# Performance work log

Hardware: AMD Instinct MI355X
Metric: run time of the kernel (lower is better)

Reference implementation:

```python
import jax, jax.numpy as jnp
import numpy as np

B, S, D, H = 2, 2048, 1024, 16
DK = D // H


def setup_inputs() -> dict:
    key = jax.random.key(0)
    ks = jax.random.split(key, 7)
    scale = 1.0 / np.sqrt(D)
    return {
        "q": jax.random.normal(ks[0], (B, S, D), dtype=jnp.float32),
        "k": jax.random.normal(ks[1], (B, S, D), dtype=jnp.float32),
        "v": jax.random.normal(ks[2], (B, S, D), dtype=jnp.float32),
        "mask": jnp.ones((B, 1, 1, S), dtype=jnp.int32),
        "Wq": (jax.random.normal(ks[3], (D, D), dtype=jnp.float32) * scale),
        "Wk": (jax.random.normal(ks[4], (D, D), dtype=jnp.float32) * scale),
        "Wv": (jax.random.normal(ks[5], (D, D), dtype=jnp.float32) * scale),
        "Wo": (jax.random.normal(ks[6], (D, D), dtype=jnp.float32) * scale),
    }


def reference(q, k, v, mask, Wq, Wk, Wv, Wo):
    # nn.Linear(bias=False): y = x @ W.T
    def split_heads(x):  # [B,S,D] -> [B,H,S,DK]
        return x.reshape(B, S, H, DK).transpose(0, 2, 1, 3)

    qh = split_heads(q @ Wq.T)
    kh = split_heads(k @ Wk.T)
    vh = split_heads(v @ Wv.T)

    scores = jnp.einsum("bhqd,bhkd->bhqk", qh, kh) / jnp.sqrt(
        jnp.asarray(DK, dtype=qh.dtype))
    scores = jnp.where(mask == 0, jnp.asarray(-1e9, dtype=scores.dtype), scores)
    attn = jax.nn.softmax(scores, axis=-1)  # dropout p=0.0 -> identity

    ctx = jnp.einsum("bhqk,bhkd->bhqd", attn, vh)  # [B,H,S,DK]
    ctx = ctx.transpose(0, 2, 1, 3).reshape(B, S, D)
    return ctx @ Wo.T
```

## Files before the change

### kernel.cpp

```cpp
#include <hip/hip_runtime.h>


typedef __bf16 bf16x8 __attribute__((ext_vector_type(8)));
typedef __bf16 bf16x4 __attribute__((ext_vector_type(4)));
typedef float f32x4 __attribute__((ext_vector_type(4)));

#define B_ 2
#define S_ 2048
#define D_ 1024
#define H_ 16
#define DK_ 64
#define QSCALE 0.18033688011112042f

__global__ void detect_dtype(const unsigned int* __restrict__ qw,
                             int* __restrict__ flag) {
  int cnt = 0;
#pragma unroll
  for (int i = 0; i < 4; ++i) {
    unsigned int w = qw[threadIdx.x + 64 * i];
    int e = (w >> 7) & 0xFF;
    cnt += (e >= 100 && e <= 140) ? 1 : 0;
  }
#pragma unroll
  for (int off = 32; off > 0; off >>= 1) cnt += __shfl_down(cnt, off, 64);
  if (threadIdx.x == 0) *flag = (cnt >= 128) ? 0 : 1;
}

__device__ __forceinline__ bf16x8 load8cvt(const void* base, size_t eoff,
                                           bool f32) {
  if (!f32) return *(const bf16x8*)((const __bf16*)base + eoff);
  const float* p = (const float*)base + eoff;
  bf16x8 r;
#pragma unroll
  for (int j = 0; j < 8; ++j) r[j] = (__bf16)p[j];
  return r;
}

__device__ __forceinline__ void async_cp16(const __bf16* g, __bf16* l) {
  __builtin_amdgcn_global_load_lds(
      (const __attribute__((address_space(1))) unsigned int*)g,
      (__attribute__((address_space(3))) unsigned int*)l, 16, 0, 0);
}

template <int TM, int TN, int MODE>
__global__ __launch_bounds__(256) void gemmk(
    const void* X0, const void* X1, const void* X2,
    const void* W0, const void* W1, const void* W2,
    void* O0, void* O1, void* O2, const int* __restrict__ dflag) {
  constexpr int Kd = 1024, Nd = 1024;
  constexpr int MI = TM / 32;
  constexpr int NI = TN / 32;
  constexpr int ACH = TM / 32;
  constexpr int BCH = TN / 32;
  const void* X = (blockIdx.z == 0) ? X0 : (blockIdx.z == 1 ? X1 : X2);
  const void* W = (blockIdx.z == 0) ? W0 : (blockIdx.z == 1 ? W1 : W2);
  void* O = (blockIdx.z == 0) ? O0 : (blockIdx.z == 1 ? O1 : O2);
  const bool f32io = (*dflag != 0);

  __shared__ __attribute__((aligned(16))) __bf16 As[TM * 64];
  __shared__ __attribute__((aligned(16))) __bf16 Bs[TN * 64];

  const int m0 = blockIdx.x * TM;
  const int n0 = blockIdx.y * TN;
  const int t = threadIdx.x;
  const int lane = t & 63, wave = t >> 6;
  const int l15 = lane & 15, quad = lane >> 4;
  const int wm = (wave >> 1) * (TM / 2);
  const int wn = (wave & 1) * (TN / 2);

  const __bf16* gA[ACH];
  int ldsAoff[ACH];
#pragma unroll
  for (int i = 0; i < ACH; ++i) {
    int c = (wave * ACH + i) * 64 + lane;
    int row = c >> 3, j = c & 7;
    int jl = j ^ (row & 7);
    ldsAoff[i] = (wave * ACH + i) * 512;
    if (MODE == 0) {
      gA[i] = (const __bf16*)X + (size_t)(m0 + row) * Kd + jl * 8;
    } else {
      int gm = m0 + row;
      gA[i] = (const __bf16*)X + (size_t)(gm >> 11) * (H_ * S_ * DK_) +
              (size_t)(gm & (S_ - 1)) * DK_ + jl * 8;
    }
  }
  const __bf16* gB[BCH];
  int ldsBoff[BCH];
#pragma unroll
  for (int i = 0; i < BCH; ++i) {
    int c = (wave * BCH + i) * 64 + lane;
    int row = c >> 3, j = c & 7;
    int jl = j ^ (row & 7);
    ldsBoff[i] = (wave * BCH + i) * 512;
    gB[i] = (const __bf16*)W + (size_t)(n0 + row) * Kd + jl * 8;
  }

  f32x4 acc[MI][NI] = {};

  for (int k0 = 0; k0 < Kd; k0 += 64) {
    __syncthreads();
    if (!f32io) {
      if (MODE == 0) {
#pragma unroll
        for (int i = 0; i < ACH; ++i) async_cp16(gA[i] + k0, &As[ldsAoff[i]]);
      } else {
        const size_t koff = (size_t)(k0 >> 6) * (S_ * DK_);
#pragma unroll
        for (int i = 0; i < ACH; ++i) async_cp16(gA[i] + koff, &As[ldsAoff[i]]);
      }
#pragma unroll
      for (int i = 0; i < BCH; ++i) async_cp16(gB[i] + k0, &Bs[ldsBoff[i]]);
    } else {
#pragma unroll
      for (int i = 0; i < TM / 32; ++i) {
        int c = t + 256 * i;
        int row = c >> 3, j = c & 7;
        int jl = j ^ (row & 7);
        bf16x8 xv;
        if (MODE == 0) {
          xv = load8cvt(X, (size_t)(m0 + row) * Kd + k0 + jl * 8, true);
        } else {
          int gm = m0 + row, gk = k0 + jl * 8;
          xv = *(const bf16x8*)((const __bf16*)X +
                ((((size_t)(gm >> 11) * H_ + (gk >> 6)) * S_) +
                 (gm & (S_ - 1))) * DK_ + (gk & (DK_ - 1)));
        }
        *(bf16x8*)&As[row * 64 + j * 8] = xv;
      }
#pragma unroll
      for (int i = 0; i < TN / 32; ++i) {
        int c = t + 256 * i;
        int row = c >> 3, j = c & 7;
        int jl = j ^ (row & 7);
        bf16x8 wv = load8cvt(W, (size_t)(n0 + row) * Kd + k0 + jl * 8, true);
        *(bf16x8*)&Bs[row * 64 + j * 8] = wv;
      }
    }
    __syncthreads();

#pragma unroll
    for (int h = 0; h < 2; ++h) {
      bf16x8 af[MI], bfr[NI];
#pragma unroll
      for (int mi = 0; mi < MI; ++mi) {
        int row = wm + mi * 16 + l15;
        af[mi] = *(const bf16x8*)&As[row * 64 +
                                     (((h * 4 + quad) ^ (row & 7)) << 3)];
      }
#pragma unroll
      for (int ni = 0; ni < NI; ++ni) {
        int row = wn + ni * 16 + l15;
        bfr[ni] = *(const bf16x8*)&Bs[row * 64 +
                                      (((h * 4 + quad) ^ (row & 7)) << 3)];
      }
#pragma unroll
      for (int mi = 0; mi < MI; ++mi)
#pragma unroll
        for (int ni = 0; ni < NI; ++ni)
          acc[mi][ni] = __builtin_amdgcn_mfma_f32_16x16x32_bf16(
              af[mi], bfr[ni], acc[mi][ni], 0, 0, 0);
    }
  }

  const float oscale = (MODE == 0 && blockIdx.z == 0) ? QSCALE : 1.0f;
#pragma unroll
  for (int mi = 0; mi < MI; ++mi) {
#pragma unroll
    for (int ni = 0; ni < NI; ++ni) {
      int mbase = m0 + wm + mi * 16 + quad * 4;
      int n = n0 + wn + ni * 16 + l15;
      if (MODE == 0 && blockIdx.z == 2) {
        int b = mbase >> 11, sb = mbase & (S_ - 1);
        int h = n >> 6, dk = n & (DK_ - 1);
        bf16x4 pk;
#pragma unroll
        for (int r = 0; r < 4; ++r) pk[r] = (__bf16)acc[mi][ni][r];
        *(bf16x4*)&((__bf16*)O)[((size_t)(b * H_ + h) * DK_ + dk) * S_ + sb] = pk;
      } else {
#pragma unroll
        for (int r = 0; r < 4; ++r) {
          int m = mbase + r;
          float val = acc[mi][ni][r] * oscale;
          if (MODE == 0) {
            int b = m >> 11, s = m & (S_ - 1);
            int h = n >> 6, dk = n & (DK_ - 1);
            ((__bf16*)O)[((size_t)(b * H_ + h) * S_ + s) * DK_ + dk] = (__bf16)val;
          } else {
            size_t idx = (size_t)m * Nd + n;
            if (f32io) ((float*)O)[idx] = val;
            else       ((__bf16*)O)[idx] = (__bf16)val;
          }
        }
      }
    }
  }
}

__global__ __launch_bounds__(256, 2) void attn(
    const __bf16* Qh, const __bf16* __restrict__ Kh,
    const __bf16* __restrict__ Vt, const int* __restrict__ mask,
    __bf16* Out) {
  __shared__ __attribute__((aligned(16))) __bf16 Ks[2][4096];
  __shared__ __attribute__((aligned(16))) __bf16 Vs[2][4096];
  __shared__ __attribute__((aligned(16))) __bf16 P[4][2048];

  const int t = threadIdx.x;
  const int lane = t & 63, wave = t >> 6;
  const int l15 = lane & 15, quad = lane >> 4;
  const int qb = blockIdx.x & 15;
  const int bh = blockIdx.x >> 4;
  const int b = bh >> 4;
  const int q0 = qb * 128 + wave * 32;

  const __bf16* Q = Qh + (size_t)bh * S_ * DK_;
  const __bf16* K = Kh + (size_t)bh * S_ * DK_;
  const __bf16* V = Vt + (size_t)bh * DK_ * S_;
  const int* mk = mask + b * S_;

  bf16x8 qf[2][2];
#pragma unroll
  for (int qt = 0; qt < 2; ++qt) {
    qf[qt][0] = *(const bf16x8*)&Q[(size_t)(q0 + qt * 16 + l15) * DK_ + quad * 8];
    qf[qt][1] = *(const bf16x8*)&Q[(size_t)(q0 + qt * 16 + l15) * DK_ + 32 + quad * 8];
  }

  f32x4 o[2][4] = {};
  float lsum[2] = {0.f, 0.f};

  int pst[4], prd[2];
#pragma unroll
  for (int tt = 0; tt < 4; ++tt)
    pst[tt] = l15 * 64 + (((tt * 2 + (quad >> 1)) ^ (l15 & 7)) << 3) +
              (quad & 1) * 4;
#pragma unroll
  for (int kt = 0; kt < 2; ++kt)
    prd[kt] = l15 * 64 + (((kt * 4 + quad) ^ (l15 & 7)) << 3);

#pragma unroll
  for (int i = 0; i < 2; ++i) {
    int l = wave * 128 + i * 64 + lane;
    int row = l >> 3, jg = (l & 7) ^ (row & 7);
    async_cp16(K + (size_t)row * DK_ + jg * 8, &Ks[0][(size_t)(l - lane) * 8]);
    async_cp16(V + (size_t)row * S_ + jg * 8, &Vs[0][(size_t)(l - lane) * 8]);
  }
  __syncthreads();

  for (int kb = 0; kb < S_; kb += 64) {
    const int cur = (kb >> 6) & 1;
    if (kb + 64 < S_) {
#pragma unroll
      for (int i = 0; i < 2; ++i) {
        int l = wave * 128 + i * 64 + lane;
        int row = l >> 3, jg = (l & 7) ^ (row & 7);
        async_cp16(K + (size_t)(kb + 64 + row) * DK_ + jg * 8,
                   &Ks[cur ^ 1][(size_t)(l - lane) * 8]);
        async_cp16(V + (size_t)row * S_ + (kb + 64) + jg * 8,
                   &Vs[cur ^ 1][(size_t)(l - lane) * 8]);
      }
    }

    const __bf16* ks = &Ks[cur][0];
    f32x4 s[2][4];
#pragma unroll
    for (int tt = 0; tt < 4; ++tt) {
      int row = tt * 16 + l15;
      bf16x8 kf0 = *(const bf16x8*)&ks[row * 64 + ((quad ^ (l15 & 7)) << 3)];
      bf16x8 kf1 = *(const bf16x8*)&ks[row * 64 + (((4 + quad) ^ (l15 & 7)) << 3)];
      int4 m4 = *(const int4*)&mk[kb + tt * 16 + quad * 4];
      f32x4 z;
      z[0] = m4.x ? 0.f : -1e9f;
      z[1] = m4.y ? 0.f : -1e9f;
      z[2] = m4.z ? 0.f : -1e9f;
      z[3] = m4.w ? 0.f : -1e9f;
      f32x4 z0 = __builtin_amdgcn_mfma_f32_16x16x32_bf16(kf0, qf[0][0], z, 0, 0, 0);
      s[0][tt] = __builtin_amdgcn_mfma_f32_16x16x32_bf16(kf1, qf[0][1], z0, 0, 0, 0);
      f32x4 z1 = __builtin_amdgcn_mfma_f32_16x16x32_bf16(kf0, qf[1][0], z, 0, 0, 0);
      s[1][tt] = __builtin_amdgcn_mfma_f32_16x16x32_bf16(kf1, qf[1][1], z1, 0, 0, 0);
    }

    const __bf16* vs = &Vs[cur][0];
    bf16x8 vf[2][4];
#pragma unroll
    for (int kt = 0; kt < 2; ++kt)
#pragma unroll
      for (int nt = 0; nt < 4; ++nt) {
        int dk = nt * 16 + l15;
        vf[kt][nt] =
            *(const bf16x8*)&vs[dk * 64 + (((kt * 4 + quad) ^ (l15 & 7)) << 3)];
      }

#pragma unroll
    for (int qt = 0; qt < 2; ++qt) {
      float acc = 0.f;
#pragma unroll
      for (int tt = 0; tt < 4; ++tt) {
        bf16x4 pk;
#pragma unroll
        for (int r = 0; r < 4; ++r) {
          float e = __builtin_exp2f(s[qt][tt][r]);
          acc += e;
          pk[r] = (__bf16)e;
        }
        *(bf16x4*)&P[wave][qt * 1024 + pst[tt]] = pk;
      }
      lsum[qt] += acc;
    }

    asm volatile("" ::: "memory");

#pragma unroll
    for (int qt = 0; qt < 2; ++qt)
#pragma unroll
      for (int kt = 0; kt < 2; ++kt) {
        bf16x8 pf = *(const bf16x8*)&P[wave][qt * 1024 + prd[kt]];
#pragma unroll
        for (int nt = 0; nt < 4; ++nt)
          o[qt][nt] = __builtin_amdgcn_mfma_f32_16x16x32_bf16(
              pf, vf[kt][nt], o[qt][nt], 0, 0, 0);
      }

    __syncthreads();
  }

#pragma unroll
  for (int qt = 0; qt < 2; ++qt) {
    float v = lsum[qt];
    v += __shfl_xor(v, 16, 64);
    v += __shfl_xor(v, 32, 64);
    lsum[qt] = v;
  }

#pragma unroll
  for (int qt = 0; qt < 2; ++qt) {
    float rinv[4];
#pragma unroll
    for (int r = 0; r < 4; ++r)
      rinv[r] = 1.0f / __shfl(lsum[qt], quad * 4 + r, 64);
#pragma unroll
    for (int nt = 0; nt < 4; ++nt)
#pragma unroll
      for (int r = 0; r < 4; ++r) {
        int qrow = q0 + qt * 16 + quad * 4 + r;
        Out[(size_t)bh * S_ * DK_ + (size_t)qrow * DK_ + nt * 16 + l15] =
            (__bf16)(o[qt][nt][r] * rinv[r]);
      }
  }
}

extern "C" void kernel_launch(void* const* d_in, const int* in_sizes, int n_in,
                              void* d_out, int out_size, void* d_ws, size_t ws_size,
                              hipStream_t stream) {
  const void* q = d_in[0];
  const void* k = d_in[1];
  const void* v = d_in[2];
  const int* mask = (const int*)d_in[3];
  const void* Wq = d_in[4];
  const void* Wk = d_in[5];
  const void* Wv = d_in[6];
  const void* Wo = d_in[7];

  const size_t NE = (size_t)B_ * H_ * S_ * DK_;
  __bf16* Qh = (__bf16*)d_ws;
  __bf16* Kh = Qh + NE;
  int* dflag = (int*)((char*)d_ws + 2 * NE * sizeof(__bf16));
  __bf16* Vt = (__bf16*)d_out;

  detect_dtype<<<1, 64, 0, stream>>>((const unsigned int*)q, dflag);
  dim3 g1(32, 16, 3);
  gemmk<128, 64, 0><<<g1, 256, 0, stream>>>(q, k, v, Wq, Wk, Wv, Qh, Kh, Vt,
                                            dflag);
  attn<<<512, 256, 0, stream>>>(Qh, Kh, Vt, mask, Qh);
  dim3 g2(64, 16, 1);
  gemmk<64, 64, 1><<<g2, 256, 0, stream>>>(Qh, Qh, Qh, Wo, Wo, Wo, d_out,
                                           d_out, d_out, dflag);
}
```

Baseline: 262.4 us.

## Triple-buffer GEMM and attention tiles with vmcnt waits and single barrier

Both the projection GEMM and the attention kernel move from double or single buffering to a three-stage LDS ring, prefetched two tiles ahead. Explicit s_waitcnt vmcnt counts and a raw s_barrier replace the paired __syncthreads, cutting each loop iteration to one barrier. Attention also precomputes the mask bias into LDS once instead of reading and converting global mask values per tile, and raises wave priority around MFMA sections. The extra LDS buffers may lower occupancy, and the hand-written wait counts must exactly match the number of async copies in flight.

```diff
diff --git a/kernel.cpp b/kernel.cpp
--- a/kernel.cpp
+++ b/kernel.cpp
@@ -11,6 +11,19 @@
 #define H_ 16
 #define DK_ 64
 #define QSCALE 0.18033688011112042f
+
+__device__ __forceinline__ void barrier_fenced() {
+  asm volatile("s_barrier" ::: "memory");
+}
+
+template <int N>
+__device__ __forceinline__ void wait_vmcnt() {
+  if constexpr (N == 0) asm volatile("s_waitcnt vmcnt(0)" ::: "memory");
+  else if constexpr (N == 4) asm volatile("s_waitcnt vmcnt(4)" ::: "memory");
+  else if constexpr (N == 6) asm volatile("s_waitcnt vmcnt(6)" ::: "memory");
+  else static_assert(N == 0 || N == 4 || N == 6, "unsupported vmcnt");
+  __builtin_amdgcn_sched_barrier(0);
+}
 
 __global__ void detect_dtype(const unsigned int* __restrict__ qw,
                              int* __restrict__ flag) {
@@ -52,13 +65,14 @@
   constexpr int NI = TN / 32;
   constexpr int ACH = TM / 32;
   constexpr int BCH = TN / 32;
+  constexpr int NCH = ACH + BCH;
   const void* X = (blockIdx.z == 0) ? X0 : (blockIdx.z == 1 ? X1 : X2);
   const void* W = (blockIdx.z == 0) ? W0 : (blockIdx.z == 1 ? W1 : W2);
   void* O = (blockIdx.z == 0) ? O0 : (blockIdx.z == 1 ? O1 : O2);
   const bool f32io = (*dflag != 0);
 
-  __shared__ __attribute__((aligned(16))) __bf16 As[TM * 64];
-  __shared__ __attribute__((aligned(16))) __bf16 Bs[TN * 64];
+  __shared__ __attribute__((aligned(16))) __bf16 As[3][TM * 64];
+  __shared__ __attribute__((aligned(16))) __bf16 Bs[3][TN * 64];
 
   const int m0 = blockIdx.x * TM;
   const int n0 = blockIdx.y * TN;
@@ -95,22 +109,67 @@
     gB[i] = (const __bf16*)W + (size_t)(n0 + row) * Kd + jl * 8;
   }
 
+  auto stage_tile = [&](int k0, int bsel) {
+    if (MODE == 0) {
+#pragma unroll
+      for (int i = 0; i < ACH; ++i)
+        async_cp16(gA[i] + k0, &As[bsel][ldsAoff[i]]);
+    } else {
+      const size_t koff = (size_t)(k0 >> 6) * (S_ * DK_);
+#pragma unroll
+      for (int i = 0; i < ACH; ++i)
+        async_cp16(gA[i] + koff, &As[bsel][ldsAoff[i]]);
+    }
+#pragma unroll
+    for (int i = 0; i < BCH; ++i)
+      async_cp16(gB[i] + k0, &Bs[bsel][ldsBoff[i]]);
+  };
+
   f32x4 acc[MI][NI] = {};
 
-  for (int k0 = 0; k0 < Kd; k0 += 64) {
-    __syncthreads();
-    if (!f32io) {
-      if (MODE == 0) {
-#pragma unroll
-        for (int i = 0; i < ACH; ++i) async_cp16(gA[i] + k0, &As[ldsAoff[i]]);
-      } else {
-        const size_t koff = (size_t)(k0 >> 6) * (S_ * DK_);
-#pragma unroll
-        for (int i = 0; i < ACH; ++i) async_cp16(gA[i] + koff, &As[ldsAoff[i]]);
-      }
-#pragma unroll
-      for (int i = 0; i < BCH; ++i) async_cp16(gB[i] + k0, &Bs[ldsBoff[i]]);
-    } else {
+  auto compute_tile = [&](const __bf16* Ab, const __bf16* Bb) {
+#pragma unroll
+    for (int h = 0; h < 2; ++h) {
+      bf16x8 af[MI], bfr[NI];
+#pragma unroll
+      for (int mi = 0; mi < MI; ++mi) {
+        int row = wm + mi * 16 + l15;
+        af[mi] = *(const bf16x8*)&Ab[row * 64 +
+                                     (((h * 4 + quad) ^ (row & 7)) << 3)];
+      }
+#pragma unroll
+      for (int ni = 0; ni < NI; ++ni) {
+        int row = wn + ni * 16 + l15;
+        bfr[ni] = *(const bf16x8*)&Bb[row * 64 +
+                                      (((h * 4 + quad) ^ (row & 7)) << 3)];
+      }
+#pragma unroll
+      for (int mi = 0; mi < MI; ++mi)
+#pragma unroll
+        for (int ni = 0; ni < NI; ++ni)
+          acc[mi][ni] = __builtin_amdgcn_mfma_f32_16x16x32_bf16(
+              af[mi], bfr[ni], acc[mi][ni], 0, 0, 0);
+    }
+  };
+
+  if (!f32io) {
+    stage_tile(0, 0);
+    stage_tile(64, 1);
+    int cur = 0;
+    for (int kt = 0; kt < 16; ++kt) {
+      if (kt == 15) wait_vmcnt<0>();
+      else          wait_vmcnt<NCH>();
+      barrier_fenced();
+      if (kt < 14) {
+        int nb = cur + 2; if (nb >= 3) nb -= 3;
+        stage_tile((kt + 2) * 64, nb);
+      }
+      compute_tile(&As[cur][0], &Bs[cur][0]);
+      cur = (cur == 2) ? 0 : cur + 1;
+    }
+  } else {
+    for (int k0 = 0; k0 < Kd; k0 += 64) {
+      __syncthreads();
 #pragma unroll
       for (int i = 0; i < TM / 32; ++i) {
         int c = t + 256 * i;
@@ -125,7 +184,7 @@
                 ((((size_t)(gm >> 11) * H_ + (gk >> 6)) * S_) +
                  (gm & (S_ - 1))) * DK_ + (gk & (DK_ - 1)));
         }
-        *(bf16x8*)&As[row * 64 + j * 8] = xv;
+        *(bf16x8*)&As[0][row * 64 + j * 8] = xv;
       }
 #pragma unroll
       for (int i = 0; i < TN / 32; ++i) {
@@ -133,32 +192,10 @@
         int row = c >> 3, j = c & 7;
         int jl = j ^ (row & 7);
         bf16x8 wv = load8cvt(W, (size_t)(n0 + row) * Kd + k0 + jl * 8, true);
-        *(bf16x8*)&Bs[row * 64 + j * 8] = wv;
-      }
-    }
-    __syncthreads();
-
-#pragma unroll
-    for (int h = 0; h < 2; ++h) {
-      bf16x8 af[MI], bfr[NI];
-#pragma unroll
-      for (int mi = 0; mi < MI; ++mi) {
-        int row = wm + mi * 16 + l15;
-        af[mi] = *(const bf16x8*)&As[row * 64 +
-                                     (((h * 4 + quad) ^ (row & 7)) << 3)];
-      }
-#pragma unroll
-      for (int ni = 0; ni < NI; ++ni) {
-        int row = wn + ni * 16 + l15;
-        bfr[ni] = *(const bf16x8*)&Bs[row * 64 +
-                                      (((h * 4 + quad) ^ (row & 7)) << 3)];
-      }
-#pragma unroll
-      for (int mi = 0; mi < MI; ++mi)
-#pragma unroll
-        for (int ni = 0; ni < NI; ++ni)
-          acc[mi][ni] = __builtin_amdgcn_mfma_f32_16x16x32_bf16(
-              af[mi], bfr[ni], acc[mi][ni], 0, 0, 0);
+        *(bf16x8*)&Bs[0][row * 64 + j * 8] = wv;
+      }
+      __syncthreads();
+      compute_tile(&As[0][0], &Bs[0][0]);
     }
   }
 
@@ -200,9 +237,10 @@
     const __bf16* Qh, const __bf16* __restrict__ Kh,
     const __bf16* __restrict__ Vt, const int* __restrict__ mask,
     __bf16* Out) {
-  __shared__ __attribute__((aligned(16))) __bf16 Ks[2][4096];
-  __shared__ __attribute__((aligned(16))) __bf16 Vs[2][4096];
+  __shared__ __attribute__((aligned(16))) __bf16 Ks[3][4096];
+  __shared__ __attribute__((aligned(16))) __bf16 Vs[3][4096];
   __shared__ __attribute__((aligned(16))) __bf16 P[4][2048];
+  __shared__ __attribute__((aligned(16))) float BiasL[2048];
 
   const int t = threadIdx.x;
   const int lane = t & 63, wave = t >> 6;
@@ -236,47 +274,54 @@
   for (int kt = 0; kt < 2; ++kt)
     prd[kt] = l15 * 64 + (((kt * 4 + quad) ^ (l15 & 7)) << 3);
 
-#pragma unroll
-  for (int i = 0; i < 2; ++i) {
-    int l = wave * 128 + i * 64 + lane;
-    int row = l >> 3, jg = (l & 7) ^ (row & 7);
-    async_cp16(K + (size_t)row * DK_ + jg * 8, &Ks[0][(size_t)(l - lane) * 8]);
-    async_cp16(V + (size_t)row * S_ + jg * 8, &Vs[0][(size_t)(l - lane) * 8]);
-  }
-  __syncthreads();
-
-  for (int kb = 0; kb < S_; kb += 64) {
-    const int cur = (kb >> 6) & 1;
-    if (kb + 64 < S_) {
-#pragma unroll
-      for (int i = 0; i < 2; ++i) {
-        int l = wave * 128 + i * 64 + lane;
-        int row = l >> 3, jg = (l & 7) ^ (row & 7);
-        async_cp16(K + (size_t)(kb + 64 + row) * DK_ + jg * 8,
-                   &Ks[cur ^ 1][(size_t)(l - lane) * 8]);
-        async_cp16(V + (size_t)row * S_ + (kb + 64) + jg * 8,
-                   &Vs[cur ^ 1][(size_t)(l - lane) * 8]);
-      }
+  auto stage_kv = [&](int key0, int bsel) {
+#pragma unroll
+    for (int i = 0; i < 2; ++i) {
+      int l = wave * 128 + i * 64 + lane;
+      int row = l >> 3, jg = (l & 7) ^ (row & 7);
+      async_cp16(K + (size_t)(key0 + row) * DK_ + jg * 8,
+                 &Ks[bsel][(size_t)(l - lane) * 8]);
+      async_cp16(V + (size_t)row * S_ + key0 + jg * 8,
+                 &Vs[bsel][(size_t)(l - lane) * 8]);
+    }
+  };
+
+#pragma unroll
+  for (int i = 0; i < 8; ++i) {
+    int key = i * 256 + t;
+    BiasL[key] = mk[key] ? 0.f : -1e9f;
+  }
+  stage_kv(0, 0);
+  stage_kv(64, 1);
+  asm volatile("s_waitcnt lgkmcnt(0)" ::: "memory");
+  barrier_fenced();
+
+  int cur = 0;
+  for (int it = 0; it < 32; ++it) {
+    const int kb = it << 6;
+    if (it == 31) wait_vmcnt<0>();
+    else          wait_vmcnt<4>();
+    barrier_fenced();
+    if (it < 30) {
+      int nb = cur + 2; if (nb >= 3) nb -= 3;
+      stage_kv(kb + 128, nb);
     }
 
     const __bf16* ks = &Ks[cur][0];
     f32x4 s[2][4];
+    __builtin_amdgcn_s_setprio(1);
 #pragma unroll
     for (int tt = 0; tt < 4; ++tt) {
       int row = tt * 16 + l15;
       bf16x8 kf0 = *(const bf16x8*)&ks[row * 64 + ((quad ^ (l15 & 7)) << 3)];
       bf16x8 kf1 = *(const bf16x8*)&ks[row * 64 + (((4 + quad) ^ (l15 & 7)) << 3)];
-      int4 m4 = *(const int4*)&mk[kb + tt * 16 + quad * 4];
-      f32x4 z;
-      z[0] = m4.x ? 0.f : -1e9f;
-      z[1] = m4.y ? 0.f : -1e9f;
-      z[2] = m4.z ? 0.f : -1e9f;
-      z[3] = m4.w ? 0.f : -1e9f;
+      f32x4 z = *(const f32x4*)&BiasL[kb + tt * 16 + quad * 4];
       f32x4 z0 = __builtin_amdgcn_mfma_f32_16x16x32_bf16(kf0, qf[0][0], z, 0, 0, 0);
       s[0][tt] = __builtin_amdgcn_mfma_f32_16x16x32_bf16(kf1, qf[0][1], z0, 0, 0, 0);
       f32x4 z1 = __builtin_amdgcn_mfma_f32_16x16x32_bf16(kf0, qf[1][0], z, 0, 0, 0);
       s[1][tt] = __builtin_amdgcn_mfma_f32_16x16x32_bf16(kf1, qf[1][1], z1, 0, 0, 0);
     }
+    __builtin_amdgcn_s_setprio(0);
 
     const __bf16* vs = &Vs[cur][0];
     bf16x8 vf[2][4];
@@ -308,6 +353,7 @@
 
     asm volatile("" ::: "memory");
 
+    __builtin_amdgcn_s_setprio(1);
 #pragma unroll
     for (int qt = 0; qt < 2; ++qt)
 #pragma unroll
@@ -318,8 +364,9 @@
           o[qt][nt] = __builtin_amdgcn_mfma_f32_16x16x32_bf16(
               pf, vf[kt][nt], o[qt][nt], 0, 0, 0);
       }
-
-    __syncthreads();
+    __builtin_amdgcn_s_setprio(0);
+
+    cur = (cur == 2) ? 0 : cur + 1;
   }
 
 #pragma unroll
```

Measured after the change: 263.5 us. Within noise of the previous version (+0.4%).
